# Kernel tuning notes

Measured on AMD Instinct MI355X. Metric: run time of the kernel, lower is better.

Reference implementation:

```python
import jax, jax.numpy as jnp
import numpy as np

B, N, F, E, K, R, H = 16, 2048, 2048, 128, 10, 2, 2


def setup_inputs() -> dict:
    key = jax.random.key(0)
    ks = jax.random.split(key, 11)
    s = 0.1  # keep embeddings close so the Gaussian kernel does not underflow
    rel = jax.random.normal(ks[0], (B, E), jnp.float32) * s
    arg1 = jax.random.normal(ks[1], (B, E), jnp.float32) * s
    arg2 = jax.random.normal(ks[2], (B, E), jnp.float32) * s
    fact_rel = jax.random.normal(ks[3], (B, F, E), jnp.float32) * s
    fact_arg1 = jax.random.normal(ks[4], (B, F, E), jnp.float32) * s
    fact_arg2 = jax.random.normal(ks[5], (B, F, E), jnp.float32) * s
    entity_embeddings = jax.random.normal(ks[6], (B, N, E), jnp.float32) * s
    hop_W = jax.random.normal(ks[7], (R, H, E, E), jnp.float32) / jnp.sqrt(jnp.float32(E))
    hop_b = jax.random.normal(ks[8], (R, H, E), jnp.float32) * 0.01
    nb_facts = jax.random.randint(ks[9], (B,), F // 2, F + 1, jnp.int32)
    nb_entities = jax.random.randint(ks[10], (B,), N // 2, N + 1, jnp.int32)
    return dict(rel=rel, arg1=arg1, arg2=arg2, fact_rel=fact_rel,
                fact_arg1=fact_arg1, fact_arg2=fact_arg2,
                entity_embeddings=entity_embeddings, hop_W=hop_W, hop_b=hop_b,
                nb_facts=nb_facts, nb_entities=nb_entities)


def reference(rel, arg1, arg2, fact_rel, fact_arg1, fact_arg2,
              entity_embeddings, hop_W, hop_b, nb_facts, nb_entities):
    # Gaussian kernel k(x,y) = exp(-||x-y||^2 / 2), batched: x [B,T,E], y [B,F,E] -> [B,T,F]
    def kern(x, y):
        d2 = (jnp.sum(x * x, -1)[:, :, None] + jnp.sum(y * y, -1)[:, None, :]
              - 2.0 * jnp.einsum('bte,bfe->btf', x, y))
        return jnp.exp(-0.5 * d2)

    fact_mask = (jnp.arange(F) < nb_facts[:, None])[:, None, :]            # [B,1,F]
    ent_mask = (jnp.arange(N) < nb_entities[:, None]).astype(rel.dtype)    # [B,N]

    # BatchNeuralKB.score: max over (valid) facts of product of kernels. [B,T,E]x3 -> [B,T]
    def model_score(r, a1, a2):
        s = kern(r, fact_rel) * kern(a1, fact_arg1) * kern(a2, fact_arg2)  # [B,T,F]
        return jnp.max(jnp.where(fact_mask, s, 0.0), axis=-1)

    # BatchNeuralKB.forward, (s,p,?) -> score per candidate object entity. [B,1,E] -> [B,N]
    def forward_sp(r, a1):
        kr = jnp.where(fact_mask, kern(r, fact_rel) * kern(a1, fact_arg1), 0.0)  # [B,1,F]
        kE = kern(entity_embeddings, fact_arg2)                                  # [B,N,F]
        return jnp.max(kr * kE, axis=-1) * ent_mask                              # [B,N]

    # (?,p,o) -> score per candidate subject entity
    def forward_po(r, a2):
        kr = jnp.where(fact_mask, kern(r, fact_rel) * kern(a2, fact_arg2), 0.0)
        kE = kern(entity_embeddings, fact_arg1)
        return jnp.max(kr * kE, axis=-1) * ent_mask

    # r_score(depth=1) = max(depth_r_score(0), depth_r_score(1))
    # depth_r_score(0) == model.score
    scores_0 = model_score(rel[:, None], arg1[:, None], arg2[:, None])[:, 0]  # [B]

    global_res = None
    for r_idx in range(R):
        is_rev = (r_idx % 2 == 1)
        # LinearReformulator: hop relations from rel
        h1 = rel @ hop_W[r_idx, 0] + hop_b[r_idx, 0]  # [B,E]
        h2 = rel @ hop_W[r_idx, 1] + hop_b[r_idx, 1]
        # hop 1: r_hop -> scores over all entities, then top-k beam
        if is_rev:
            sp = forward_po(h1[:, None], arg1[:, None])  # [B,N]
        else:
            sp = forward_sp(h1[:, None], arg1[:, None])
        z_scores, z_idx = jax.lax.top_k(sp, K)                                  # [B,K]
        z_emb = jnp.take_along_axis(entity_embeddings, z_idx[:, :, None], axis=1)  # [B,K,E]
        # final hop: r_score(depth=0) == model.score with branched args
        h2k = jnp.broadcast_to(h2[:, None, :], (B, K, E))
        a2k = jnp.broadcast_to(arg2[:, None, :], (B, K, E))
        if is_rev:
            s2 = model_score(h2k, a2k, z_emb)  # [B,K]
        else:
            s2 = model_score(h2k, z_emb, a2k)
        rule_scores = jnp.minimum(s2, z_scores)   # tnorm = 'min'
        rule_res = jnp.max(rule_scores, axis=1)   # max over branches [B]
        global_res = rule_res if global_res is None else jnp.maximum(global_res, rule_res)

    return jnp.maximum(scores_0, global_res)
```

## Files before the change

kernel.cpp:

```cpp
#include <hip/hip_runtime.h>
#include <math.h>

#define Bb 16
#define Nn 2048
#define Ff 2048
#define Ee 128
#define Kk 10
#define S2FC 8
#define S2F (Ff / S2FC)

typedef __attribute__((ext_vector_type(8))) short short8;
typedef __attribute__((ext_vector_type(4))) float f32x4;
typedef unsigned int u32;

__device__ inline float wave_sum(float x) {
    for (int o = 32; o; o >>= 1) x += __shfl_down(x, o);
    return x;
}

__device__ inline void bsplit(float x, unsigned short& h, unsigned short& l) {
    unsigned int u = __float_as_uint(x);
    h = (unsigned short)(u >> 16);
    float hf = __uint_as_float(u & 0xFFFF0000u);
    l = (unsigned short)(__float_as_uint(x - hf) >> 16);
}

__device__ inline void atomic_fmax_pos(float* addr, float v) {
    atomicMax((unsigned int*)addr, __float_as_uint(v));
}

__device__ inline void gload_lds16(const void* g, void* l) {
    __builtin_amdgcn_global_load_lds(
        (const __attribute__((address_space(1))) u32*)g,
        (__attribute__((address_space(3))) u32*)l, 16, 0, 0);
}


__global__ __launch_bounds__(256) void k_pfe(
    const float* __restrict__ rel, const float* __restrict__ arg1,
    const float* __restrict__ arg2, const float* __restrict__ frel,
    const float* __restrict__ fa1, const float* __restrict__ fa2,
    const float* __restrict__ ent, const float* __restrict__ hop_W,
    const float* __restrict__ hop_b, const int* __restrict__ nb_facts,
    unsigned short* __restrict__ B0, unsigned short* __restrict__ B1,
    float* __restrict__ ent_norm, float* __restrict__ c0, float* __restrict__ c1,
    float* __restrict__ s2b0, float* __restrict__ s2b1,
    float* __restrict__ sp0, float* __restrict__ sp1, float* __restrict__ out) {
    int bx = blockIdx.x;
    int tid = threadIdx.x;
    if (bx < 128) {
        int fcb = bx & 7, b = bx >> 3;
        int nbf = nb_facts[b];
        if (fcb * 256 >= nbf) {
            int f = fcb * 256 + tid;
            size_t o = (size_t)b * Ff + f;
            const float NI = -INFINITY;
            c0[o] = NI; c1[o] = NI; s2b0[o] = NI; s2b1[o] = NI;
            return;
        }
        __shared__ float q[7][Ee];
        __shared__ float bred[4];
        if (tid < 128) {
            q[0][tid] = rel[b * Ee + tid];
            q[1][tid] = arg1[b * Ee + tid];
            q[2][tid] = arg2[b * Ee + tid];
        }
        __syncthreads();
        {
            int e = tid & 127, hf = tid >> 7;
            const float* W0 = hop_W + (size_t)(hf * 2) * Ee * Ee;
            const float* W1 = W0 + (size_t)Ee * Ee;
            float a0 = hop_b[(hf * 2) * Ee + e];
            float a1 = hop_b[(hf * 2 + 1) * Ee + e];
            for (int qq = 0; qq < Ee; ++qq) {
                float rq = q[0][qq];
                a0 += rq * W0[qq * Ee + e];
                a1 += rq * W1[qq * Ee + e];
            }
            q[3 + hf][e] = a0;
            q[5 + hf][e] = a1;
        }
        __syncthreads();

        int f = fcb * 256 + tid;
        const float* pr = frel + ((size_t)b * Ff + f) * Ee;
        const float* p1 = fa1 + ((size_t)b * Ff + f) * Ee;
        const float* p2 = fa2 + ((size_t)b * Ff + f) * Ee;
        float d_rr = 0, d_a11 = 0, d_a22 = 0, d_h10 = 0, d_h11 = 0, d_h20 = 0, d_h21 = 0;
        float d_a12 = 0, d_a21 = 0, n1 = 0, n2 = 0;
#pragma unroll 8
        for (int e0 = 0; e0 < Ee; e0 += 4) {
            float4 vr4 = *(const float4*)(pr + e0);
            float4 v14 = *(const float4*)(p1 + e0);
            float4 v24 = *(const float4*)(p2 + e0);
            const float* vrp = (const float*)&vr4;
            const float* v1p = (const float*)&v14;
            const float* v2p = (const float*)&v24;
#pragma unroll
            for (int j = 0; j < 4; ++j) {
                int e = e0 + j;
                float fr = vrp[j], f1 = v1p[j], f2 = v2p[j];
                float t;
                t = q[0][e] - fr; d_rr  += t * t;
                t = q[1][e] - f1; d_a11 += t * t;
                t = q[2][e] - f2; d_a22 += t * t;
                t = q[3][e] - fr; d_h10 += t * t;
                t = q[4][e] - fr; d_h11 += t * t;
                t = q[5][e] - fr; d_h20 += t * t;
                t = q[6][e] - fr; d_h21 += t * t;
                t = q[1][e] - f2; d_a12 += t * t;
                t = q[2][e] - f1; d_a21 += t * t;
                n1 += f1 * f1; n2 += f2 * f2;
            }
        }
        bool valid = f < nbf;
        const float NI = -INFINITY;
        size_t o = (size_t)b * Ff + f;
        c0[o]   = valid ? (-0.5f * (d_h10 + d_a11 + n2)) : NI;
        c1[o]   = valid ? (-0.5f * (d_h11 + d_a12 + n1)) : NI;
        s2b0[o] = valid ? (-0.5f * (d_h20 + d_a22)) : NI;
        s2b1[o] = valid ? (-0.5f * (d_h21 + d_a21)) : NI;
        float lsc = valid ? (-0.5f * (d_rr + d_a11 + d_a22)) : NI;
        for (int m = 32; m; m >>= 1) lsc = fmaxf(lsc, __shfl_down(lsc, m));
        if ((tid & 63) == 0) bred[tid >> 6] = lsc;
        __syncthreads();
        if (tid == 0) {
            float m = fmaxf(fmaxf(bred[0], bred[1]), fmaxf(bred[2], bred[3]));
            atomic_fmax_pos(out + b, expf(m));
        }
    } else if (bx < 128 + 4096) {
        __shared__ uint4 tlds[16 * 33];
        int bxx = bx - 128;
        int y = bxx >> 11, bxi = bxx & 2047;
        int oct = tid & 15, fl = tid >> 4;
        int b = bxi >> 7, fbase = (bxi & 127) * 16;
        const float* src = (y == 0) ? fa2 : fa1;
        const float* s = src + ((size_t)b * Ff + fbase + fl) * Ee + oct * 8;
        float4 v0 = *(const float4*)s;
        float4 v1 = *(const float4*)(s + 4);
        float xs[8] = {v0.x, v0.y, v0.z, v0.w, v1.x, v1.y, v1.z, v1.w};
        unsigned short hi[8], lo[8];
#pragma unroll
        for (int j = 0; j < 8; ++j) bsplit(xs[j], hi[j], lo[j]);
        uint4 ph, pl;
        ph.x = (unsigned)hi[0] | ((unsigned)hi[1] << 16);
        ph.y = (unsigned)hi[2] | ((unsigned)hi[3] << 16);
        ph.z = (unsigned)hi[4] | ((unsigned)hi[5] << 16);
        ph.w = (unsigned)hi[6] | ((unsigned)hi[7] << 16);
        pl.x = (unsigned)lo[0] | ((unsigned)lo[1] << 16);
        pl.y = (unsigned)lo[2] | ((unsigned)lo[3] << 16);
        pl.z = (unsigned)lo[4] | ((unsigned)lo[5] << 16);
        pl.w = (unsigned)lo[6] | ((unsigned)lo[7] << 16);
        tlds[fl * 33 + oct * 2]     = ph;
        tlds[fl * 33 + oct * 2 + 1] = pl;
        __syncthreads();
        int F4 = (fbase >> 4) & 1, F5 = (fbase >> 5) & 1;
        unsigned char* ob = (unsigned char*)((y == 0) ? B0 : B1) +
                            (((size_t)b << 20) + (size_t)(fbase >> 6) * 32768 +
                             F5 * 4096 + F4 * 2048);
#pragma unroll
        for (int uu = 0; uu < 2; ++uu) {
            int u = tid + uu * 256;
            int fl2 = u & 15, qd = (u >> 4) & 3, p = (u >> 6) & 1, ks = u >> 7;
            *(uint4*)(ob + ks * 8192 + p * 1024 + qd * 256 + fl2 * 16) =
                tlds[fl2 * 33 + (ks * 4 + qd) * 2 + p];
        }
    } else {
        int row  = (bx - (128 + 4096)) * 4 + (tid >> 6);
        int lane = tid & 63;
        const float* p = ent + (size_t)row * Ee;
        float a = p[lane], c = p[lane + 64];
        float s = wave_sum(a * a + c * c);
        if (lane == 0) {
            ent_norm[row] = s;
            sp0[row] = 0.0f;
            sp1[row] = 0.0f;
        }
    }
}

#define BMs 256

__global__ __launch_bounds__(512, 2) void k_spmax_mfma(
    const float* __restrict__ ent, const unsigned short* __restrict__ B0,
    const unsigned short* __restrict__ B1, const float* __restrict__ c0,
    const float* __restrict__ c1, const float* __restrict__ ent_norm,
    const int* __restrict__ nb_facts, const int* __restrict__ nb_entities,
    float* __restrict__ sp0, float* __restrict__ sp1) {
    int bid = blockIdx.x;
    int br = bid & 31, nblk = bid >> 5;
    int b = br >> 1, r = br & 1;
    const unsigned short* Bt = (r == 0) ? B0 : B1;
    const float* cb = ((r == 0) ? c0 : c1) + (size_t)b * Ff;
    float* sp = ((r == 0) ? sp0 : sp1) + (size_t)b * Nn;

    int tid = threadIdx.x;
    int ne = nb_entities[b];
    if (nblk * BMs >= ne) return;
    int nch = (nb_facts[b] + 63) >> 6;

    __shared__ uint4 ldsB4[4 * 2048];
    __shared__ float ldsC[Ff];

    int wave = tid >> 6, lane = tid & 63;
    int wm = wave >> 1, wn = wave & 1;
    int lane15 = lane & 15, quad = lane >> 4;

    short8 ah[4][4], al[4][4];
    {
        const float* abase = ent + ((size_t)b * Nn + (size_t)nblk * BMs + wm * 64) * Ee;
#pragma unroll
        for (int i = 0; i < 4; ++i)
#pragma unroll
            for (int ks = 0; ks < 4; ++ks) {
                const float* p = abase + (size_t)(i * 16 + lane15) * Ee + ks * 32 + quad * 8;
                float4 v0 = *(const float4*)p;
                float4 v1 = *(const float4*)(p + 4);
                float xs[8] = {v0.x, v0.y, v0.z, v0.w, v1.x, v1.y, v1.z, v1.w};
                short8 hi8, lo8;
#pragma unroll
                for (int j = 0; j < 8; ++j) {
                    unsigned short hh, ll;
                    bsplit(xs[j], hh, ll);
                    hi8[j] = (short)hh;
                    lo8[j] = (short)ll;
                }
                ah[i][ks] = hi8;
                al[i][ks] = lo8;
            }
    }

    unsigned char* ldsB = (unsigned char*)ldsB4;
    const unsigned char* gB = (const unsigned char*)Bt + ((size_t)b << 20);

#define STAGE(cc)                                                              \
    {                                                                          \
        const unsigned char* gc_ = gB + (size_t)(cc) * 32768;                  \
        unsigned char* lb_ = ldsB + ((cc) & 3) * 32768;                        \
        _Pragma("unroll")                                                      \
        for (int t_ = 0; t_ < 4; ++t_) {                                       \
            int seg_ = t_ * 8 + wave;                                          \
            gload_lds16(gc_ + seg_ * 1024 + (lane << 4), lb_ + seg_ * 1024);   \
        }                                                                      \
    }

    ((float4*)ldsC)[tid] = ((const float4*)cb)[tid];
    STAGE(0);
    STAGE(1);
    __syncthreads();

    float mmax[4][4];
#pragma unroll
    for (int i = 0; i < 4; ++i)
#pragma unroll
        for (int rr = 0; rr < 4; ++rr) mmax[i][rr] = -INFINITY;

    for (int c = 0; c < nch; ++c) {
        if (c + 2 < nch) STAGE(c + 2);
        __builtin_amdgcn_sched_barrier(0);
        if (c + 2 < nch)      asm volatile("s_waitcnt vmcnt(8)" ::: "memory");
        else if (c + 1 < nch) asm volatile("s_waitcnt vmcnt(4)" ::: "memory");
        else                  asm volatile("s_waitcnt vmcnt(0)" ::: "memory");
        __builtin_amdgcn_sched_barrier(0);
        __builtin_amdgcn_s_barrier();
        __builtin_amdgcn_sched_barrier(0);

        float cj0 = ldsC[c * 64 + wn * 32 + lane15];
        float cj1 = ldsC[c * 64 + wn * 32 + 16 + lane15];
        f32x4 acc[4][2];
#pragma unroll
        for (int i = 0; i < 4; ++i) {
            acc[i][0] = (f32x4){cj0, cj0, cj0, cj0};
            acc[i][1] = (f32x4){cj1, cj1, cj1, cj1};
        }
        const unsigned char* bb = ldsB + (c & 3) * 32768 + wn * 4096 + (lane << 4);
#pragma unroll
        for (int ks = 0; ks < 4; ++ks) {
            const unsigned char* bk = bb + ks * 8192;
            short8 bh0 = *(const short8*)(bk);
            short8 bl0 = *(const short8*)(bk + 1024);
            short8 bh1 = *(const short8*)(bk + 2048);
            short8 bl1 = *(const short8*)(bk + 3072);
#pragma unroll
            for (int i = 0; i < 4; ++i) {
                acc[i][0] = __builtin_amdgcn_mfma_f32_16x16x32_bf16(ah[i][ks], bh0, acc[i][0], 0, 0, 0);
                acc[i][0] = __builtin_amdgcn_mfma_f32_16x16x32_bf16(al[i][ks], bh0, acc[i][0], 0, 0, 0);
                acc[i][0] = __builtin_amdgcn_mfma_f32_16x16x32_bf16(ah[i][ks], bl0, acc[i][0], 0, 0, 0);
                acc[i][1] = __builtin_amdgcn_mfma_f32_16x16x32_bf16(ah[i][ks], bh1, acc[i][1], 0, 0, 0);
                acc[i][1] = __builtin_amdgcn_mfma_f32_16x16x32_bf16(al[i][ks], bh1, acc[i][1], 0, 0, 0);
                acc[i][1] = __builtin_amdgcn_mfma_f32_16x16x32_bf16(ah[i][ks], bl1, acc[i][1], 0, 0, 0);
            }
        }

#pragma unroll
        for (int j = 0; j < 2; ++j)
#pragma unroll
            for (int i = 0; i < 4; ++i)
#pragma unroll
                for (int rr = 0; rr < 4; ++rr)
                    mmax[i][rr] = fmaxf(mmax[i][rr], acc[i][j][rr]);
    }
#undef STAGE

    __syncthreads();
    float* red = (float*)ldsB;
#pragma unroll
    for (int i = 0; i < 4; ++i)
#pragma unroll
        for (int rr = 0; rr < 4; ++rr) {
            float v = mmax[i][rr];
#pragma unroll
            for (int m = 1; m < 16; m <<= 1) v = fmaxf(v, __shfl_xor(v, m));
            if (lane15 == 0) red[(wm * 64 + i * 16 + quad * 4 + rr) * 2 + wn] = v;
        }
    __syncthreads();
    if (tid < BMs) {
        float m = fmaxf(red[tid * 2], red[tid * 2 + 1]);
        int n = nblk * BMs + tid;
        if (n < ne)
            sp[n] = expf(m - 0.5f * ent_norm[(size_t)b * Nn + n]);
    }
}

__global__ __launch_bounds__(256) void k_s2t(
    const float* __restrict__ ent, const float* __restrict__ fa1,
    const float* __restrict__ fa2, const float* __restrict__ s2b0,
    const float* __restrict__ s2b1, const float* __restrict__ sp0,
    const float* __restrict__ sp1, const int* __restrict__ nb_facts,
    float* __restrict__ out) {
    int fc = blockIdx.x, b = blockIdx.y, r = blockIdx.z;
    if (fc * S2F >= nb_facts[b]) return;
    const float* factX = (r == 0) ? fa1 : fa2;
    const float* s2b   = ((r == 0) ? s2b0 : s2b1) + (size_t)b * Ff;
    const float* sp    = ((r == 0) ? sp0 : sp1) + (size_t)b * Nn;

    __shared__ float zsc[Kk];
    __shared__ int   zidx[Kk];
    __shared__ float zsh[Kk][Ee];
    __shared__ float znorm[Kk];
    __shared__ float red[4][Kk];
    __shared__ float rules[Kk];

    int tid = threadIdx.x;
    int wv = tid >> 6, lane = tid & 63;

    if (wv == 0) {
        float v[Nn / 64];
#pragma unroll
        for (int i = 0; i < Nn / 64; ++i) v[i] = sp[i * 64 + lane];
        for (int k = 0; k < Kk; ++k) {
            float best = -INFINITY; int bidx = 0;
#pragma unroll
            for (int i = 0; i < Nn / 64; ++i)
                if (v[i] > best) { best = v[i]; bidx = i * 64 + lane; }
#pragma unroll
            for (int m = 1; m < 64; m <<= 1) {
                float ov = __shfl_xor(best, m);
                int oi = __shfl_xor(bidx, m);
                if (ov > best || (ov == best && oi < bidx)) { best = ov; bidx = oi; }
            }
            if (lane == 0) { zsc[k] = best; zidx[k] = bidx; }
            if ((bidx & 63) == lane) {
                int slot = bidx >> 6;
#pragma unroll
                for (int i = 0; i < Nn / 64; ++i)
                    if (i == slot) v[i] = -INFINITY;
            }
        }
    }
    __syncthreads();
    for (int idx = tid; idx < Kk * Ee; idx += 256) {
        int k = idx >> 7, e = idx & 127;
        zsh[k][e] = ent[((size_t)b * Nn + zidx[k]) * Ee + e];
    }
    __syncthreads();
    if (tid < Kk) {
        float s = 0.f;
        for (int e = 0; e < Ee; ++e) { float v = zsh[tid][e]; s += v * v; }
        znorm[tid] = s;
    }
    __syncthreads();

    int f = fc * S2F + tid;
    const float* fp = factX + ((size_t)b * Ff + f) * Ee;
    float acc[Kk];
#pragma unroll
    for (int k = 0; k < Kk; ++k) acc[k] = 0.f;
    float nf = 0.f;
#pragma unroll 4
    for (int e0 = 0; e0 < Ee; e0 += 4) {
        float4 v = *(const float4*)(fp + e0);
        nf += v.x * v.x + v.y * v.y + v.z * v.z + v.w * v.w;
#pragma unroll
        for (int k = 0; k < Kk; ++k) {
            float4 z = *(const float4*)&zsh[k][e0];
            acc[k] += z.x * v.x + z.y * v.y + z.z * v.z + z.w * v.w;
        }
    }
    float base = s2b[f] - 0.5f * nf;
    float sc[Kk];
#pragma unroll
    for (int k = 0; k < Kk; ++k) sc[k] = base + acc[k] - 0.5f * znorm[k];
    for (int o = 32; o; o >>= 1)
#pragma unroll
        for (int k = 0; k < Kk; ++k) sc[k] = fmaxf(sc[k], __shfl_down(sc[k], o));
    if ((tid & 63) == 0)
#pragma unroll
        for (int k = 0; k < Kk; ++k) red[wv][k] = sc[k];
    __syncthreads();
    if (tid < Kk) {
        float m = fmaxf(fmaxf(red[0][tid], red[1][tid]), fmaxf(red[2][tid], red[3][tid]));
        rules[tid] = fminf(expf(m), zsc[tid]);
    }
    __syncthreads();
    if (tid == 0) {
        float g = rules[0];
#pragma unroll
        for (int k = 1; k < Kk; ++k) g = fmaxf(g, rules[k]);
        atomic_fmax_pos(out + b, g);
    }
}

extern "C" void kernel_launch(void* const* d_in, const int* in_sizes, int n_in,
                              void* d_out, int out_size, void* d_ws, size_t ws_size,
                              hipStream_t stream) {
    const float* rel  = (const float*)d_in[0];
    const float* arg1 = (const float*)d_in[1];
    const float* arg2 = (const float*)d_in[2];
    const float* frel = (const float*)d_in[3];
    const float* fa1  = (const float*)d_in[4];
    const float* fa2  = (const float*)d_in[5];
    const float* ent  = (const float*)d_in[6];
    const float* hopW = (const float*)d_in[7];
    const float* hopb = (const float*)d_in[8];
    const int* nb_facts    = (const int*)d_in[9];
    const int* nb_entities = (const int*)d_in[10];
    float* out = (float*)d_out;

    float* ws = (float*)d_ws;
    size_t off = 0;
    float* c0       = ws + off; off += (size_t)Bb * Ff;
    float* c1       = ws + off; off += (size_t)Bb * Ff;
    float* s2b0     = ws + off; off += (size_t)Bb * Ff;
    float* s2b1     = ws + off; off += (size_t)Bb * Ff;
    float* sp0      = ws + off; off += (size_t)Bb * Nn;
    float* sp1      = ws + off; off += (size_t)Bb * Nn;
    float* ent_norm = ws + off; off += (size_t)Bb * Nn;
    off = (off + 7) & ~(size_t)7;
    unsigned short* B0 = (unsigned short*)(ws + off); off += (size_t)Bb * 16 * Ff * 8;
    unsigned short* B1 = (unsigned short*)(ws + off); off += (size_t)Bb * 16 * Ff * 8;

    hipMemsetAsync(d_out, 0, (size_t)out_size * sizeof(float), stream);
    k_pfe<<<dim3(128 + 4096 + Bb * Nn / 4), 256, 0, stream>>>(
        rel, arg1, arg2, frel, fa1, fa2, ent, hopW, hopb, nb_facts,
        B0, B1, ent_norm, c0, c1, s2b0, s2b1, sp0, sp1, out);
    k_spmax_mfma<<<dim3(32 * 8), 512, 0, stream>>>(ent, B0, B1, c0, c1, ent_norm,
                                                   nb_facts, nb_entities, sp0, sp1);
    k_s2t<<<dim3(S2FC, Bb, 2), 256, 0, stream>>>(ent, fa1, fa2, s2b0, s2b1,
                                                 sp0, sp1, nb_facts, out);
}
```

Baseline: 226.4 us.

## Split fact chunks across two blocks per tile with atomic max merge

Each (batch, relation, entity-block) tile of the spmax MFMA kernel is now handled by two blocks, each taking alternating 64-fact chunks, which doubles the grid to 512 blocks. Results are merged into sp with an atomic float max. To fit more blocks per CU, the LDS ring shrinks from four to two buffers and the occupancy hint goes from 2 to 4. The prefetch/barrier schedule is reworked for the two-buffer ring and the MFMA section runs at raised wave priority. The aim is to fill more CUs on a kernel whose 256-block grid underfills the GPU, at the cost of a shallower prefetch pipeline, atomics, and duplicated A-fragment loading.

Result: slower. 388.2 us (+71.5%).

```diff
diff --git a/kernel.cpp b/kernel.cpp
--- a/kernel.cpp
+++ b/kernel.cpp
@@ -181,14 +181,17 @@
 
 #define BMs 256
 
-__global__ __launch_bounds__(512, 2) void k_spmax_mfma(
+__global__ __launch_bounds__(512, 4) void k_spmax_mfma(
     const float* __restrict__ ent, const unsigned short* __restrict__ B0,
     const unsigned short* __restrict__ B1, const float* __restrict__ c0,
     const float* __restrict__ c1, const float* __restrict__ ent_norm,
     const int* __restrict__ nb_facts, const int* __restrict__ nb_entities,
     float* __restrict__ sp0, float* __restrict__ sp1) {
     int bid = blockIdx.x;
-    int br = bid & 31, nblk = bid >> 5;
+    int h = bid >> 8;
+    int s = bid & 255;
+    if (h) s = 255 - s;
+    int br = s & 31, nblk = s >> 5;
     int b = br >> 1, r = br & 1;
     const unsigned short* Bt = (r == 0) ? B0 : B1;
     const float* cb = ((r == 0) ? c0 : c1) + (size_t)b * Ff;
@@ -198,8 +201,9 @@
     int ne = nb_entities[b];
     if (nblk * BMs >= ne) return;
     int nch = (nb_facts[b] + 63) >> 6;
-
-    __shared__ uint4 ldsB4[4 * 2048];
+    int nt = (nch - h + 1) >> 1;
+
+    __shared__ uint4 ldsB4[2 * 2048];
     __shared__ float ldsC[Ff];
 
     int wave = tid >> 6, lane = tid & 63;
@@ -233,10 +237,10 @@
     unsigned char* ldsB = (unsigned char*)ldsB4;
     const unsigned char* gB = (const unsigned char*)Bt + ((size_t)b << 20);
 
-#define STAGE(cc)                                                              \
+#define STAGE(cc, bf)                                                          \
     {                                                                          \
         const unsigned char* gc_ = gB + (size_t)(cc) * 32768;                  \
-        unsigned char* lb_ = ldsB + ((cc) & 3) * 32768;                        \
+        unsigned char* lb_ = ldsB + (bf) * 32768;                              \
         _Pragma("unroll")                                                      \
         for (int t_ = 0; t_ < 4; ++t_) {                                       \
             int seg_ = t_ * 8 + wave;                                          \
@@ -245,8 +249,8 @@
     }
 
     ((float4*)ldsC)[tid] = ((const float4*)cb)[tid];
-    STAGE(0);
-    STAGE(1);
+    STAGE(h, 0);
+    STAGE(h + 2, 1);
     __syncthreads();
 
     float mmax[4][4];
@@ -255,25 +259,18 @@
 #pragma unroll
         for (int rr = 0; rr < 4; ++rr) mmax[i][rr] = -INFINITY;
 
-    for (int c = 0; c < nch; ++c) {
-        if (c + 2 < nch) STAGE(c + 2);
-        __builtin_amdgcn_sched_barrier(0);
-        if (c + 2 < nch)      asm volatile("s_waitcnt vmcnt(8)" ::: "memory");
-        else if (c + 1 < nch) asm volatile("s_waitcnt vmcnt(4)" ::: "memory");
-        else                  asm volatile("s_waitcnt vmcnt(0)" ::: "memory");
-        __builtin_amdgcn_sched_barrier(0);
-        __builtin_amdgcn_s_barrier();
-        __builtin_amdgcn_sched_barrier(0);
-
-        float cj0 = ldsC[c * 64 + wn * 32 + lane15];
-        float cj1 = ldsC[c * 64 + wn * 32 + 16 + lane15];
+    for (int t = 0; t < nt; ++t) {
+        int cc = h + 2 * t;
+        float cj0 = ldsC[cc * 64 + wn * 32 + lane15];
+        float cj1 = ldsC[cc * 64 + wn * 32 + 16 + lane15];
         f32x4 acc[4][2];
 #pragma unroll
         for (int i = 0; i < 4; ++i) {
             acc[i][0] = (f32x4){cj0, cj0, cj0, cj0};
             acc[i][1] = (f32x4){cj1, cj1, cj1, cj1};
         }
-        const unsigned char* bb = ldsB + (c & 3) * 32768 + wn * 4096 + (lane << 4);
+        const unsigned char* bb = ldsB + (t & 1) * 32768 + wn * 4096 + (lane << 4);
+        __builtin_amdgcn_s_setprio(1);
 #pragma unroll
         for (int ks = 0; ks < 4; ++ks) {
             const unsigned char* bk = bb + ks * 8192;
@@ -291,6 +288,7 @@
                 acc[i][1] = __builtin_amdgcn_mfma_f32_16x16x32_bf16(ah[i][ks], bl1, acc[i][1], 0, 0, 0);
             }
         }
+        __builtin_amdgcn_s_setprio(0);
 
 #pragma unroll
         for (int j = 0; j < 2; ++j)
@@ -299,6 +297,19 @@
 #pragma unroll
                 for (int rr = 0; rr < 4; ++rr)
                     mmax[i][rr] = fmaxf(mmax[i][rr], acc[i][j][rr]);
+
+        __builtin_amdgcn_sched_barrier(0);
+        __builtin_amdgcn_s_barrier();
+        __builtin_amdgcn_sched_barrier(0);
+        if (t + 2 < nt) STAGE(h + 2 * (t + 2), (t & 1));
+        if (t + 1 < nt) {
+            __builtin_amdgcn_sched_barrier(0);
+            if (t + 2 < nt) asm volatile("s_waitcnt vmcnt(4)" ::: "memory");
+            else            asm volatile("s_waitcnt vmcnt(0)" ::: "memory");
+            __builtin_amdgcn_sched_barrier(0);
+            __builtin_amdgcn_s_barrier();
+            __builtin_amdgcn_sched_barrier(0);
+        }
     }
 #undef STAGE
 
@@ -318,7 +329,7 @@
         float m = fmaxf(red[tid * 2], red[tid * 2 + 1]);
         int n = nblk * BMs + tid;
         if (n < ne)
-            sp[n] = expf(m - 0.5f * ent_norm[(size_t)b * Nn + n]);
+            atomic_fmax_pos(&sp[n], expf(m - 0.5f * ent_norm[(size_t)b * Nn + n]));
     }
 }
 
@@ -454,8 +465,8 @@
     k_pfe<<<dim3(128 + 4096 + Bb * Nn / 4), 256, 0, stream>>>(
         rel, arg1, arg2, frel, fa1, fa2, ent, hopW, hopb, nb_facts,
         B0, B1, ent_norm, c0, c1, s2b0, s2b1, sp0, sp1, out);
-    k_spmax_mfma<<<dim3(32 * 8), 512, 0, stream>>>(ent, B0, B1, c0, c1, ent_norm,
-                                                   nb_facts, nb_entities, sp0, sp1);
+    k_spmax_mfma<<<dim3(512), 512, 0, stream>>>(ent, B0, B1, c0, c1, ent_norm,
+                                                nb_facts, nb_entities, sp0, sp1);
     k_s2t<<<dim3(S2FC, Bb, 2), 256, 0, stream>>>(ent, fa1, fa2, s2b0, s2b1,
                                                  sp0, sp1, nb_facts, out);
 }
```
